# Optimization experiments

Hardware: AMD Instinct MI355X
Metric: run time of the kernel (lower is better)

Reference implementation:

```python
import jax, jax.numpy as jnp
from jax import lax
import numpy as np

POOLING_COUNTS = [15, 8, 8, 8]
N = 128          # segment_num
GROUPS = 4       # GroupNorm groups
TOPK = 5
NMS_THRESH = 0.5
EPS = 1e-5


def _build_structure(pooling_counts, n):
    """Static (numpy) replication of SparseMaxPool's mask2d and pooling schedule."""
    mask2d = np.zeros((n, n), dtype=bool)
    mask2d[np.arange(n), np.arange(n)] = True
    kinds = ['k2'] * pooling_counts[0]
    for c in pooling_counts[1:]:
        kinds += ['k3'] + ['k2'] * (c - 1)
    steps, stride, offset, k = [], 1, 0, 0
    for c in pooling_counts:
        for _ in range(c):
            offset += stride
            i = np.arange(0, n - offset, stride)
            j = np.arange(offset, n, stride)
            mask2d[i, j] = True
            steps.append((kinds[k], i, j))
            k += 1
        stride *= 2
    return mask2d, steps


_MASK2D, _STEPS = _build_structure(POOLING_COUNTS, N)


def sparse_max_pool(x):
    # x: [B, D, N] -> map2d: [B, D, N, N]
    B, D, _ = x.shape
    d = np.arange(N)
    map2d = jnp.zeros((B, D, N, N), x.dtype).at[:, :, d, d].set(x)
    for kind, i, j in _STEPS:
        if kind == 'k2':      # MaxPool1d(kernel=2, stride=1)
            x = jnp.maximum(x[..., :-1], x[..., 1:])
        else:                 # MaxPool1d(kernel=3, stride=2)
            m = jnp.maximum(jnp.maximum(x[..., :-2], x[..., 1:-1]), x[..., 2:])
            x = m[..., ::2]
        map2d = map2d.at[:, :, i, j].set(x)
    return map2d


def group_norm(x, gamma, beta):
    B, C, H, W = x.shape
    xg = x.reshape(B, GROUPS, C // GROUPS, H, W)
    mu = xg.mean(axis=(2, 3, 4), keepdims=True)
    var = xg.var(axis=(2, 3, 4), keepdims=True)
    xn = ((xg - mu) * lax.rsqrt(var + EPS)).reshape(B, C, H, W)
    return xn * gamma[None, :, None, None] + beta[None, :, None, None]


def decode(map2d, conv1_w, gn_gamma, gn_beta, conv2_w, conv2_b):
    dn = ('NCHW', 'OIHW', 'NCHW')
    h = lax.conv_general_dilated(map2d, conv1_w, (1, 1), [(1, 1), (1, 1)], dimension_numbers=dn)
    h = jax.nn.relu(group_norm(h, gn_gamma, gn_beta))
    out = lax.conv_general_dilated(h, conv2_w, (1, 1), [(0, 0), (0, 0)], dimension_numbers=dn)
    return out + conv2_b[None, :, None, None]


def greedy_nms(moments, scores):
    # moments: [M, 2] (start, end); scores: [M]
    M = moments.shape[0]
    order = jnp.argsort(-scores)
    m = moments[order]
    starts, ends = m[:, 0], m[:, 1]
    ar = jnp.arange(M)

    def body(i, sup):
        inter = jnp.clip(jnp.minimum(ends, ends[i]) - jnp.maximum(starts, starts[i]), 0.0)
        union = jnp.maximum(ends, ends[i]) - jnp.minimum(starts, starts[i])
        iou = inter / union
        newly = (iou > NMS_THRESH) & (ar > i) & jnp.logical_not(sup[i])
        return sup | newly

    sup = lax.fori_loop(0, M - 1, body, jnp.zeros((M,), bool))
    keep = jnp.logical_not(sup)
    # first TOPK kept rows in sorted order (static shape)
    pri = jnp.where(keep, M - ar, 0)
    _, idx = lax.top_k(pri, TOPK)
    return m[idx]


def reference(fea, duration, conv1_w, gn_gamma, gn_beta, conv2_w, conv2_b):
    map2d = sparse_max_pool(fea)
    out = decode(map2d, conv1_w, gn_gamma, gn_beta, conv2_w, conv2_b)
    mask = jnp.asarray(_MASK2D, out.dtype)
    score2d = (jax.nn.sigmoid(out) * mask)[0, 0]           # [N, N]
    # score2d_to_moments_scores: nonzero of masked map == static nonzero of mask2d
    gi, gj = np.nonzero(_MASK2D)                            # row-major, matches torch.nonzero
    scores = score2d[gi, gj]                                # [M]
    dur = float(duration)
    moments = jnp.asarray(
        np.stack([gi * (dur / N), (gj + 1) * (dur / N)], axis=-1), jnp.float32
    )                                                       # [M, 2]
    return greedy_nms(moments, scores)                      # [TOPK, 2]


def setup_inputs() -> dict:
    key = jax.random.key(0)
    k0, k1, k2 = jax.random.split(key, 3)
    D = 768
    return {
        'fea': jax.random.normal(k0, (1, D, N), jnp.float32),
        'duration': 30,
        'conv1_w': jax.random.normal(k1, (D, D, 3, 3), jnp.float32) * 0.02,
        'gn_gamma': jnp.ones((D,), jnp.float32),
        'gn_beta': jnp.zeros((D,), jnp.float32),
        'conv2_w': jax.random.normal(k2, (1, D, 1, 1), jnp.float32) * 0.02,
        'conv2_b': jnp.zeros((1,), jnp.float32),
    }
```

## Files before the change

### kernel.cpp

```cpp
#include <hip/hip_runtime.h>
#include <math.h>

#define NPIX 128
#define MASKM 2548
#define NPAD 2560
#define MG   6912
#define KD   768

typedef __attribute__((ext_vector_type(8))) short bf16x8;
typedef __attribute__((ext_vector_type(4))) float f32x4;
typedef __attribute__((ext_vector_type(16))) float f32x16;
typedef __attribute__((ext_vector_type(8))) unsigned short ushort8;

static constexpr size_t OFF_QI   = 0;
static constexpr size_t OFF_QJ   = OFF_QI + NPAD * 4;
static constexpr size_t OFF_QIDX = OFF_QJ + NPAD * 4;
static constexpr size_t OFF_APIX = OFF_QIDX + 16384 * 4;
static constexpr size_t OFF_BAR  = OFF_APIX + 16384 * 4;
static constexpr size_t OFF_LIST = OFF_BAR + 128 * 4;
static constexpr size_t OFF_PART = OFF_LIST + 16384 * 4;
static constexpr size_t OFF_SC   = OFF_PART + 512 * 8 * 8;
static constexpr size_t OFF_HM   = OFF_SC + NPAD * 4;
static constexpr size_t OFF_AH   = OFF_HM + (size_t)MASKM * KD * 4;
static constexpr size_t OFF_AL   = OFF_AH + (size_t)MG * KD * 2;
static constexpr size_t OFF_BH   = OFF_AL + (size_t)MG * KD * 2;
static constexpr size_t OFF_BL   = OFF_BH + (size_t)NPAD * KD * 2;
static constexpr size_t OFF_YT   = OFF_BL + (size_t)NPAD * KD * 2;

__device__ __forceinline__ unsigned short f2bf(float f) {
    unsigned u = __float_as_uint(f);
    u = u + 0x7FFFu + ((u >> 16) & 1u);
    return (unsigned short)(u >> 16);
}
__device__ __forceinline__ float bf2f(unsigned short h) {
    return __uint_as_float(((unsigned)h) << 16);
}

__device__ __forceinline__ bool mask_allowed(int i, int d) {
    if (d == 0) return true;
    if (d <= 15) return true;
    if (d <= 31) return (d >= 17) && ((d & 1) == 1) && ((i & 1) == 0);
    if (d <= 63) return (d >= 35) && ((d & 3) == 3) && ((i & 3) == 0);
    return (d >= 71) && ((d & 7) == 7) && ((i & 7) == 0);
}
__device__ __forceinline__ bool masked_ij(int i, int j) {
    return (j >= i) && (j < NPIX) && (i >= 0) && mask_allowed(i, j - i);
}

__device__ __forceinline__ int rank_to_d(int i, int r) {
    int rem = NPIX - i;
    int c1 = rem < 16 ? rem : 16;
    if (r < c1) return r;
    r -= c1;
    int h2 = (rem - 1) < 31 ? (rem - 1) : 31;
    int c2 = (((i & 1) == 0) && h2 >= 17) ? ((h2 - 17) >> 1) + 1 : 0;
    if (r < c2) return 17 + 2 * r;
    r -= c2;
    int h3 = (rem - 1) < 63 ? (rem - 1) : 63;
    int c3 = (((i & 3) == 0) && h3 >= 35) ? ((h3 - 35) >> 2) + 1 : 0;
    if (r < c3) return 35 + 4 * r;
    r -= c3;
    return 71 + 8 * r;
}

#define PREP_LDS 37888
#define PASTR 148

__global__ __launch_bounds__(256) void k_prep(const float* __restrict__ fea,
                                              const float* __restrict__ w1,
                                              int* __restrict__ qi, int* __restrict__ qj,
                                              int* __restrict__ qidx, int* __restrict__ apix,
                                              double* __restrict__ part, int* __restrict__ bar,
                                              int* __restrict__ list,
                                              unsigned short* __restrict__ Ah,
                                              unsigned short* __restrict__ Al,
                                              unsigned short* __restrict__ Bh,
                                              unsigned short* __restrict__ Bl) {
    extern __shared__ char smp[];
    int tid = threadIdx.x;
    int bid = blockIdx.x;

    if (bid < 64) {
        int* cnt = (int*)smp;
        int* startv = cnt + NPIX;
        if (tid < NPIX) {
            int c = 0;
            for (int d = 0; tid + d < NPIX; ++d) if (mask_allowed(tid, d)) ++c;
            cnt[tid] = c;
        }
        __syncthreads();
        if (tid == 0) {
            int s = 0;
            for (int r = 0; r < NPIX; ++r) { startv[r] = s; s += cnt[r]; }
        }
        __syncthreads();
        int p = bid * 256 + tid;
        int i = p >> 7, j = p & 127;
        int q = -1;
        if (masked_ij(i, j)) {
            int d = j - i, r = 0;
            for (int dd = 0; dd < d; ++dd) r += mask_allowed(i, dd) ? 1 : 0;
            q = startv[i] + r;
            qi[q] = i; qj[q] = j;
        }
        qidx[p] = q;
        int act = 0;
        #pragma unroll
        for (int dy = -1; dy <= 1; ++dy)
            #pragma unroll
            for (int dx = -1; dx <= 1; ++dx)
                if (masked_ij(i + dy, j + dx)) act = 1;
        apix[p] = act;
        if (act) { int idx = atomicAdd(&bar[3], 1); list[idx] = p; }
        if (bid == 0 && tid < 8) part[tid] = 0.0;
    } else if (bid < 160) {
        float* tab = (float*)smp;
        int* cnt = (int*)(smp + 32768);
        int* startv = (int*)(smp + 33280);
        int cb = bid - 64, c0 = cb * 8;
        if (tid < NPIX) {
            int c = 0;
            for (int d = 0; tid + d < NPIX; ++d) if (mask_allowed(tid, d)) ++c;
            cnt[tid] = c;
        }
        __syncthreads();
        if (tid == 0) {
            int s = 0;
            for (int r = 0; r < NPIX; ++r) { startv[r] = s; s += cnt[r]; }
            startv[NPIX] = s;
        }
        for (int idx = tid; idx < 8 * NPIX; idx += 256) {
            int c = idx >> 7, x = idx & 127;
            tab[(c * 8) * 128 + x] = fea[(size_t)(c0 + c) * NPIX + x];
        }
        __syncthreads();
        for (int lvl = 1; lvl < 8; ++lvl) {
            int half = 1 << (lvl - 1), full = 1 << lvl;
            for (int idx = tid; idx < 8 * NPIX; idx += 256) {
                int c = idx >> 7, x = idx & 127;
                if (x + full <= NPIX)
                    tab[(c * 8 + lvl) * 128 + x] =
                        fmaxf(tab[(c * 8 + lvl - 1) * 128 + x],
                              tab[(c * 8 + lvl - 1) * 128 + x + half]);
            }
            __syncthreads();
        }
        for (int q = tid; q < NPAD; q += 256) {
            ushort8 vh = {}, vl = {};
            if (q < MASKM) {
                int i = 0;
                #pragma unroll
                for (int s = 64; s >= 1; s >>= 1) {
                    int cand = i + s;
                    if (cand <= 127 && startv[cand] <= q) i = cand;
                }
                int d = rank_to_d(i, q - startv[i]);
                int j = i + d;
                int len = d + 1;
                int lvl = 31 - __clz(len);
                int x2 = j + 1 - (1 << lvl);
                #pragma unroll
                for (int c = 0; c < 8; ++c) {
                    float v = fmaxf(tab[(c * 8 + lvl) * 128 + i], tab[(c * 8 + lvl) * 128 + x2]);
                    unsigned short hh = f2bf(v);
                    vh[c] = hh; vl[c] = f2bf(v - bf2f(hh));
                }
            }
            *(ushort8*)(Bh + (size_t)q * KD + c0) = vh;
            *(ushort8*)(Bl + (size_t)q * KD + c0) = vl;
        }
    } else {
        float* tile = (float*)smp;
        int pb = bid - 160;
        int co0 = (pb % 12) * 64, ci0 = ((pb / 12) % 12) * 64;
        int s = pb / 144;
        int cib = ci0 + s * 16;
        for (int idx = tid; idx < 2304; idx += 256) {
            int row = idx / 36, c4 = idx % 36;
            float4 v = *(const float4*)(w1 + (size_t)(co0 + row) * MG + cib * 9 + c4 * 4);
            *(float4*)&tile[row * PASTR + c4 * 4] = v;
        }
        __syncthreads();
        for (int idx = tid; idx < 1152; idx += 256) {
            int tap = idx / 128;
            int rem = idx - tap * 128;
            int co = rem >> 1, half = rem & 1;
            ushort8 vh, vl;
            #pragma unroll
            for (int c = 0; c < 8; ++c) {
                float v = tile[co * PASTR + (half * 8 + c) * 9 + tap];
                unsigned short hi = f2bf(v);
                vh[c] = hi;
                vl[c] = f2bf(v - bf2f(hi));
            }
            size_t ob = (size_t)(tap * 768 + co0 + co) * KD + cib + half * 8;
            *(ushort8*)(Ah + ob) = vh;
            *(ushort8*)(Al + ob) = vl;
        }
    }
}

#define BUFSZ   73728
#define SB_BH   32768

__global__ __launch_bounds__(512, 1) void k_gemm(const unsigned short* __restrict__ Ah,
                                                 const unsigned short* __restrict__ Al,
                                                 const unsigned short* __restrict__ Bh,
                                                 const unsigned short* __restrict__ Bl,
                                                 float* __restrict__ Yt) {
    extern __shared__ char sm[];
    int tid = threadIdx.x;
    int wave = tid >> 6, lane = tid & 63;

    int bid = (int)blockIdx.x;
    int xcd = bid & 7, loc = bid >> 3;
    int m0 = loc * 256, n0 = xcd * 320;

    int wm = (wave & 3) << 6, wn = (wave >> 2) * 160;
    int r32 = lane & 31, hi2 = lane >> 5;
    int rb  = (r32 >> 4) * 1024 + hi2 * 256 + (r32 & 15) * 16;
    int awb = (wm >> 4) * 1024 + rb;
    int bwb = (wn >> 4) * 1024 + rb;

    int lrow = lane & 15, lchk = lane >> 4;
    const unsigned short* sp[9];
    int so[9];
    #pragma unroll
    for (int s = 0; s < 9; ++s) {
        int gid = wave * 9 + s;
        const unsigned short* base;
        int row0, ldso;
        if (gid < 16)      { base = Ah; row0 = m0 + gid * 16;        ldso = gid * 1024; }
        else if (gid < 32) { base = Al; row0 = m0 + (gid - 16) * 16; ldso = 16384 + (gid - 16) * 1024; }
        else if (gid < 52) { base = Bh; row0 = n0 + (gid - 32) * 16; ldso = SB_BH + (gid - 32) * 1024; }
        else               { base = Bl; row0 = n0 + (gid - 52) * 16; ldso = SB_BH + 20480 + (gid - 52) * 1024; }
        sp[s] = base + (size_t)(row0 + lrow) * KD + lchk * 8;
        so[s] = ldso;
    }

    f32x16 acc[2][5] = {};
    char* CB = sm;
    char* NB = sm + BUFSZ;

    #define STAGE(DST, s, koff) __builtin_amdgcn_global_load_lds( \
        (const __attribute__((address_space(1))) unsigned int*)(sp[s] + (koff)), \
        (__attribute__((address_space(3))) unsigned int*)((DST) + so[s]), 16, 0, 0)
    #define ARD(hl, mf, ks) (*(const bf16x8*)(CB + (hl) * 16384 + awb + (mf) * 2048 + (ks) * 512))
    #define BRD(hl, nf, ks) (*(const bf16x8*)(CB + SB_BH + (hl) * 20480 + bwb + (nf) * 2048 + (ks) * 512))
    #define TRIP(mf, nf, xh, xl, yh, yl) \
        acc[mf][nf] = __builtin_amdgcn_mfma_f32_32x32x16_bf16(xh, yh, acc[mf][nf], 0, 0, 0); \
        acc[mf][nf] = __builtin_amdgcn_mfma_f32_32x32x16_bf16(xh, yl, acc[mf][nf], 0, 0, 0); \
        acc[mf][nf] = __builtin_amdgcn_mfma_f32_32x32x16_bf16(xl, yh, acc[mf][nf], 0, 0, 0);
    #define RBAR __builtin_amdgcn_s_barrier()
    #define SB0  __builtin_amdgcn_sched_barrier(0)
    #define CL6(nf, xh0, xl0, xh1, xl1, yh, yl) \
        __builtin_amdgcn_s_setprio(1); \
        TRIP(0, nf, xh0, xl0, yh, yl) \
        TRIP(1, nf, xh1, xl1, yh, yl) \
        __builtin_amdgcn_s_setprio(0);

    #pragma unroll
    for (int s = 0; s < 9; ++s) STAGE(CB, s, 0);
    __syncthreads();

    for (int t = 0; t < 24; ++t) {
        int kn = (t + 1) * 32;
        bool stg = (t < 23);
        bf16x8 a0h, a0l, a1h, a1l;
        bf16x8 c0h, c0l, c1h, c1l;
        bf16x8 bxh, bxl, byh, byl;

        a0h = ARD(0, 0, 0); a0l = ARD(1, 0, 0);
        a1h = ARD(0, 1, 0); a1l = ARD(1, 1, 0);
        bxh = BRD(0, 0, 0); bxl = BRD(1, 0, 0);
        if (stg) { STAGE(NB, 0, kn); STAGE(NB, 1, kn); STAGE(NB, 2, kn); }
        RBAR;

        byh = BRD(0, 1, 0); byl = BRD(1, 1, 0);
        SB0;
        CL6(0, a0h, a0l, a1h, a1l, bxh, bxl)
        RBAR;
        bxh = BRD(0, 2, 0); bxl = BRD(1, 2, 0);
        SB0;
        CL6(1, a0h, a0l, a1h, a1l, byh, byl)
        RBAR;
        byh = BRD(0, 3, 0); byl = BRD(1, 3, 0);
        if (stg) { STAGE(NB, 3, kn); STAGE(NB, 4, kn); }
        SB0;
        CL6(2, a0h, a0l, a1h, a1l, bxh, bxl)
        RBAR;
        bxh = BRD(0, 4, 0); bxl = BRD(1, 4, 0);
        SB0;
        CL6(3, a0h, a0l, a1h, a1l, byh, byl)
        RBAR;
        c0h = ARD(0, 0, 1); c0l = ARD(1, 0, 1);
        c1h = ARD(0, 1, 1); c1l = ARD(1, 1, 1);
        byh = BRD(0, 0, 1); byl = BRD(1, 0, 1);
        if (stg) { STAGE(NB, 5, kn); STAGE(NB, 6, kn); }
        SB0;
        CL6(4, a0h, a0l, a1h, a1l, bxh, bxl)
        RBAR;
        bxh = BRD(0, 1, 1); bxl = BRD(1, 1, 1);
        SB0;
        CL6(0, c0h, c0l, c1h, c1l, byh, byl)
        RBAR;
        byh = BRD(0, 2, 1); byl = BRD(1, 2, 1);
        if (stg) { STAGE(NB, 7, kn); STAGE(NB, 8, kn); }
        SB0;
        CL6(1, c0h, c0l, c1h, c1l, bxh, bxl)
        RBAR;
        bxh = BRD(0, 3, 1); bxl = BRD(1, 3, 1);
        SB0;
        CL6(2, c0h, c0l, c1h, c1l, byh, byl)
        RBAR;
        byh = BRD(0, 4, 1); byl = BRD(1, 4, 1);
        SB0;
        CL6(3, c0h, c0l, c1h, c1l, bxh, bxl)
        RBAR;
        CL6(4, c0h, c0l, c1h, c1l, byh, byl)

        __syncthreads();
        char* tmp = CB; CB = NB; NB = tmp;
    }

    #pragma unroll
    for (int mf = 0; mf < 2; ++mf)
        #pragma unroll
        for (int nf = 0; nf < 5; ++nf) {
            int n = n0 + wn + nf * 32 + r32;
            size_t rowb = (size_t)n * MG + m0 + wm + mf * 32 + 4 * hi2;
            #pragma unroll
            for (int g = 0; g < 4; ++g) {
                f32x4 v = { acc[mf][nf][g * 4 + 0], acc[mf][nf][g * 4 + 1],
                            acc[mf][nf][g * 4 + 2], acc[mf][nf][g * 4 + 3] };
                *(f32x4*)(Yt + rowb + 8 * g) = v;
            }
        }
    #undef STAGE
    #undef ARD
    #undef BRD
    #undef TRIP
    #undef RBAR
    #undef SB0
    #undef CL6
}

__global__ __launch_bounds__(256) void k_gather(const float* __restrict__ Yt,
                                                const int* __restrict__ qidx,
                                                const int* __restrict__ list,
                                                const int* __restrict__ bar,
                                                float* __restrict__ hm,
                                                double* __restrict__ part) {
    __shared__ double red1[256 * 4], red2[256 * 4];
    int tid = threadIdx.x;
    int wave = tid >> 6, lane = tid & 63;
    double a1[3] = {0, 0, 0}, a2[3] = {0, 0, 0};
    int gs[3];
    #pragma unroll
    for (int s = 0; s < 3; ++s) gs[s] = (64 * s + lane) / 48;

    int nact = bar[3];
    for (int wid = blockIdx.x * 4 + wave; wid < nact; wid += gridDim.x * 4) {
        int p = list[wid];
        int y = p >> 7, x = p & 127;
        float4 hv[3] = {};
        #pragma unroll
        for (int tap = 0; tap < 9; ++tap) {
            int i = y + tap / 3 - 1, j = x + tap % 3 - 1;
            if ((unsigned)i < 128u && (unsigned)j < 128u) {
                int q = qidx[i * NPIX + j];
                if (q >= 0) {
                    const float* yr = Yt + (size_t)q * MG + tap * 768 + lane * 4;
                    #pragma unroll
                    for (int s = 0; s < 3; ++s) {
                        float4 v = *(const float4*)(yr + s * 256);
                        hv[s].x += v.x; hv[s].y += v.y; hv[s].z += v.z; hv[s].w += v.w;
                    }
                }
            }
        }
        int qp = qidx[p];
        if (qp >= 0) {
            #pragma unroll
            for (int s = 0; s < 3; ++s)
                *(float4*)(hm + (size_t)qp * KD + s * 256 + lane * 4) = hv[s];
        }
        #pragma unroll
        for (int s = 0; s < 3; ++s) {
            a1[s] += (double)hv[s].x + (double)hv[s].y + (double)hv[s].z + (double)hv[s].w;
            a2[s] += (double)hv[s].x * hv[s].x + (double)hv[s].y * hv[s].y +
                     (double)hv[s].z * hv[s].z + (double)hv[s].w * hv[s].w;
        }
    }
    #pragma unroll
    for (int g = 0; g < 4; ++g) { red1[tid * 4 + g] = 0.0; red2[tid * 4 + g] = 0.0; }
    #pragma unroll
    for (int s = 0; s < 3; ++s) { red1[tid * 4 + gs[s]] = a1[s]; red2[tid * 4 + gs[s]] = a2[s]; }
    __syncthreads();
    if (tid < 8) {
        int g = tid & 3;
        double s = 0.0;
        if (tid < 4) { for (int i = 0; i < 256; ++i) s += red1[i * 4 + g]; }
        else         { for (int i = 0; i < 256; ++i) s += red2[i * 4 + g]; }
        atomicAdd(&part[tid], s);
    }
}

#define SNMS_LDS 44544

__global__ __launch_bounds__(256) void k_scorenms(const float* __restrict__ hm,
                                                  const double* __restrict__ part,
                                                  const float* __restrict__ gamma,
                                                  const float* __restrict__ beta,
                                                  const float* __restrict__ w2,
                                                  const float* __restrict__ b2,
                                                  float* __restrict__ scores,
                                                  const int* __restrict__ qi,
                                                  const int* __restrict__ qj,
                                                  const int* __restrict__ durp,
                                                  int* __restrict__ bar,
                                                  float* __restrict__ out) {
    extern __shared__ char smf[];
    int tid = threadIdx.x;
    int bid = (int)blockIdx.x;
    int lane = tid & 63;

    {
        float mu[4], rs[4];
        const double cnt = 192.0 * 16384.0;
        #pragma unroll
        for (int g = 0; g < 4; ++g) {
            double m = part[g] / cnt;
            double v = part[4 + g] / cnt - m * m;
            mu[g] = (float)m;
            rs[g] = (float)(1.0 / sqrt(v + 1e-5));
        }
        int q = bid * 4 + (tid >> 6);
        const float* hp = hm + (size_t)q * KD;
        float s = 0.f;
        for (int c = lane; c < KD; c += 64) {
            int g = c / 192;
            float v = (hp[c] - mu[g]) * rs[g] * gamma[c] + beta[c];
            s += fmaxf(v, 0.f) * w2[c];
        }
        for (int o = 32; o; o >>= 1) s += __shfl_down(s, o, 64);
        if (lane == 0) scores[q] = 1.f / (1.f + expf(-(s + b2[0])));
    }
    __syncthreads();
    if (tid == 0)
        __hip_atomic_fetch_add(&bar[2], 1, __ATOMIC_RELEASE, __HIP_MEMORY_SCOPE_AGENT);
    if (bid != 0) return;

    if (tid == 0) {
        while (__hip_atomic_load(&bar[2], __ATOMIC_RELAXED, __HIP_MEMORY_SCOPE_AGENT) < 637)
            __builtin_amdgcn_s_sleep(8);
        (void)__hip_atomic_load(&bar[2], __ATOMIC_ACQUIRE, __HIP_MEMORY_SCOPE_AGENT);
    }
    __syncthreads();

    {
        unsigned long long* key = (unsigned long long*)smf;
        float* ss = (float*)(smf + 20384);
        float* ee = (float*)(smf + 30576);
        unsigned char* st = (unsigned char*)(smf + 40768);
        unsigned long long* wm0 = (unsigned long long*)(smf + 43328);
        unsigned long long* wm1 = (unsigned long long*)(smf + 43360);
        __shared__ int sh_keeper, keepq[5];
        __shared__ float sh_s0, sh_e0;

        float delta = (float)(*durp) / 128.f;
        for (int i = tid; i < MASKM; i += 256) {
            unsigned sb = __float_as_uint(scores[i]);
            key[i] = ((unsigned long long)sb << 32) | (unsigned)(4095 - i);
            ss[i] = qi[i] * delta;
            ee[i] = (qj[i] + 1) * delta;
            st[i] = 0;
        }
        __syncthreads();
        for (int round = 0; round < 5; ++round) {
            unsigned long long b0 = 0, b1 = 0;
            for (int i = tid; i < MASKM; i += 256) {
                unsigned char s = st[i];
                unsigned long long k = key[i];
                if (s == 0) { if (k > b0) b0 = k; }
                else if (s == 1) { if (k > b1) b1 = k; }
            }
            for (int o = 32; o; o >>= 1) {
                unsigned lo0 = __shfl_down((unsigned)b0, o, 64);
                unsigned hi0 = __shfl_down((unsigned)(b0 >> 32), o, 64);
                unsigned long long u0 = ((unsigned long long)hi0 << 32) | lo0;
                unsigned lo1 = __shfl_down((unsigned)b1, o, 64);
                unsigned hi1 = __shfl_down((unsigned)(b1 >> 32), o, 64);
                unsigned long long u1 = ((unsigned long long)hi1 << 32) | lo1;
                if (u0 > b0) b0 = u0;
                if (u1 > b1) b1 = u1;
            }
            if ((tid & 63) == 0) { wm0[tid >> 6] = b0; wm1[tid >> 6] = b1; }
            __syncthreads();
            if (tid == 0) {
                unsigned long long B0 = 0, B1 = 0;
                for (int w = 0; w < 4; ++w) {
                    if (wm0[w] > B0) B0 = wm0[w];
                    if (wm1[w] > B1) B1 = wm1[w];
                }
                int keeper = (B0 != 0);
                unsigned long long B = keeper ? B0 : B1;
                int q = 4095 - (int)(B & 0xFFFFFFFFull);
                st[q] = keeper ? 2 : 3;
                sh_keeper = keeper;
                sh_s0 = ss[q]; sh_e0 = ee[q];
                keepq[round] = q;
            }
            __syncthreads();
            if (sh_keeper) {
                float s0 = sh_s0, e0 = sh_e0;
                for (int i = tid; i < MASKM; i += 256) {
                    if (st[i] == 0) {
                        float inter = fminf(ee[i], e0) - fmaxf(ss[i], s0);
                        if (inter > 0.f) {
                            float uni = fmaxf(ee[i], e0) - fminf(ss[i], s0);
                            if (inter / uni > 0.5f) st[i] = 1;
                        }
                    }
                }
            }
            __syncthreads();
        }
        if (tid < 5) { out[tid * 2] = ss[keepq[tid]]; out[tid * 2 + 1] = ee[keepq[tid]]; }
    }
}

extern "C" void kernel_launch(void* const* d_in, const int* in_sizes, int n_in,
                              void* d_out, int out_size, void* d_ws, size_t ws_size,
                              hipStream_t stream) {
    const float* fea   = (const float*)d_in[0];
    const int*   dur   = (const int*)d_in[1];
    const float* w1    = (const float*)d_in[2];
    const float* gamma = (const float*)d_in[3];
    const float* beta  = (const float*)d_in[4];
    const float* w2    = (const float*)d_in[5];
    const float* b2    = (const float*)d_in[6];
    float* out = (float*)d_out;

    char* ws = (char*)d_ws;
    int*    qi     = (int*)(ws + OFF_QI);
    int*    qj     = (int*)(ws + OFF_QJ);
    int*    qidx   = (int*)(ws + OFF_QIDX);
    int*    apix   = (int*)(ws + OFF_APIX);
    int*    bar    = (int*)(ws + OFF_BAR);
    int*    list   = (int*)(ws + OFF_LIST);
    double* part   = (double*)(ws + OFF_PART);
    float*  scores = (float*)(ws + OFF_SC);
    float*  hm     = (float*)(ws + OFF_HM);
    unsigned short* AhU = (unsigned short*)(ws + OFF_AH);
    unsigned short* AlU = (unsigned short*)(ws + OFF_AL);
    unsigned short* BhU = (unsigned short*)(ws + OFF_BH);
    unsigned short* BlU = (unsigned short*)(ws + OFF_BL);
    float*  Yt     = (float*)(ws + OFF_YT);

    static bool attr_set = false;
    if (!attr_set) {
        hipFuncSetAttribute((const void*)k_prep,
                            hipFuncAttributeMaxDynamicSharedMemorySize, PREP_LDS);
        hipFuncSetAttribute((const void*)k_gemm,
                            hipFuncAttributeMaxDynamicSharedMemorySize, 2 * BUFSZ);
        hipFuncSetAttribute((const void*)k_scorenms,
                            hipFuncAttributeMaxDynamicSharedMemorySize, SNMS_LDS);
        attr_set = true;
    }

    hipMemsetAsync(bar, 0, 16, stream);
    k_prep<<<736, 256, PREP_LDS, stream>>>(fea, w1, qi, qj, qidx, apix, part, bar,
                                           list, AhU, AlU, BhU, BlU);
    k_gemm<<<216, 512, 2 * BUFSZ, stream>>>(AhU, AlU, BhU, BlU, Yt);
    k_gather<<<1536, 256, 0, stream>>>(Yt, qidx, list, bar, hm, part);
    k_scorenms<<<637, 256, SNMS_LDS, stream>>>(hm, part, gamma, beta, w2, b2,
                                               scores, qi, qj, dur, bar, out);
}
```

Measured before the change: 240.3 us.

## Fuse gather and score/NMS kernels with a grid barrier; closed-form mask ranks

```diff
diff --git a/kernel.cpp b/kernel.cpp
--- a/kernel.cpp
+++ b/kernel.cpp
@@ -15,8 +15,7 @@
 static constexpr size_t OFF_QI   = 0;
 static constexpr size_t OFF_QJ   = OFF_QI + NPAD * 4;
 static constexpr size_t OFF_QIDX = OFF_QJ + NPAD * 4;
-static constexpr size_t OFF_APIX = OFF_QIDX + 16384 * 4;
-static constexpr size_t OFF_BAR  = OFF_APIX + 16384 * 4;
+static constexpr size_t OFF_BAR  = OFF_QIDX + 16384 * 4;
 static constexpr size_t OFF_LIST = OFF_BAR + 128 * 4;
 static constexpr size_t OFF_PART = OFF_LIST + 16384 * 4;
 static constexpr size_t OFF_SC   = OFF_PART + 512 * 8 * 8;
@@ -47,6 +46,29 @@
     return (j >= i) && (j < NPIX) && (i >= 0) && mask_allowed(i, j - i);
 }
 
+__device__ __forceinline__ int row_cnt(int i) {
+    int rem = NPIX - i;
+    int c1 = rem < 16 ? rem : 16;
+    int h2 = (rem - 1) < 31 ? (rem - 1) : 31;
+    int c2 = (((i & 1) == 0) && h2 >= 17) ? ((h2 - 17) >> 1) + 1 : 0;
+    int h3 = (rem - 1) < 63 ? (rem - 1) : 63;
+    int c3 = (((i & 3) == 0) && h3 >= 35) ? ((h3 - 35) >> 2) + 1 : 0;
+    int h4 = rem - 1;
+    int c4 = (((i & 7) == 0) && h4 >= 71) ? ((h4 - 71) >> 3) + 1 : 0;
+    return c1 + c2 + c3 + c4;
+}
+__device__ __forceinline__ int rank_fwd(int i, int d) {
+    int rem = NPIX - i;
+    int c1 = rem < 16 ? rem : 16;
+    if (d < 16) return d;
+    int h2 = (rem - 1) < 31 ? (rem - 1) : 31;
+    int c2 = (((i & 1) == 0) && h2 >= 17) ? ((h2 - 17) >> 1) + 1 : 0;
+    if (d <= 31) return c1 + ((d - 17) >> 1);
+    int h3 = (rem - 1) < 63 ? (rem - 1) : 63;
+    int c3 = (((i & 3) == 0) && h3 >= 35) ? ((h3 - 35) >> 2) + 1 : 0;
+    if (d <= 63) return c1 + c2 + ((d - 35) >> 2);
+    return c1 + c2 + c3 + ((d - 71) >> 3);
+}
 __device__ __forceinline__ int rank_to_d(int i, int r) {
     int rem = NPIX - i;
     int c1 = rem < 16 ? rem : 16;
@@ -69,7 +91,7 @@
 __global__ __launch_bounds__(256) void k_prep(const float* __restrict__ fea,
                                               const float* __restrict__ w1,
                                               int* __restrict__ qi, int* __restrict__ qj,
-                                              int* __restrict__ qidx, int* __restrict__ apix,
+                                              int* __restrict__ qidx,
                                               double* __restrict__ part, int* __restrict__ bar,
                                               int* __restrict__ list,
                                               unsigned short* __restrict__ Ah,
@@ -81,52 +103,36 @@
     int bid = blockIdx.x;
 
     if (bid < 64) {
-        int* cnt = (int*)smp;
-        int* startv = cnt + NPIX;
-        if (tid < NPIX) {
-            int c = 0;
-            for (int d = 0; tid + d < NPIX; ++d) if (mask_allowed(tid, d)) ++c;
-            cnt[tid] = c;
-        }
-        __syncthreads();
+        int* startv = (int*)smp;
         if (tid == 0) {
             int s = 0;
-            for (int r = 0; r < NPIX; ++r) { startv[r] = s; s += cnt[r]; }
+            for (int r = 0; r < NPIX; ++r) { startv[r] = s; s += row_cnt(r); }
         }
         __syncthreads();
         int p = bid * 256 + tid;
         int i = p >> 7, j = p & 127;
-        int q = -1;
         if (masked_ij(i, j)) {
-            int d = j - i, r = 0;
-            for (int dd = 0; dd < d; ++dd) r += mask_allowed(i, dd) ? 1 : 0;
-            q = startv[i] + r;
+            int q = startv[i] + rank_fwd(i, j - i);
             qi[q] = i; qj[q] = j;
-        }
-        qidx[p] = q;
+            qidx[p] = q;
+        } else {
+            qidx[p] = -1;
+        }
         int act = 0;
         #pragma unroll
         for (int dy = -1; dy <= 1; ++dy)
             #pragma unroll
             for (int dx = -1; dx <= 1; ++dx)
                 if (masked_ij(i + dy, j + dx)) act = 1;
-        apix[p] = act;
         if (act) { int idx = atomicAdd(&bar[3], 1); list[idx] = p; }
         if (bid == 0 && tid < 8) part[tid] = 0.0;
     } else if (bid < 160) {
         float* tab = (float*)smp;
-        int* cnt = (int*)(smp + 32768);
-        int* startv = (int*)(smp + 33280);
+        int* startv = (int*)(smp + 32768);
         int cb = bid - 64, c0 = cb * 8;
-        if (tid < NPIX) {
-            int c = 0;
-            for (int d = 0; tid + d < NPIX; ++d) if (mask_allowed(tid, d)) ++c;
-            cnt[tid] = c;
-        }
-        __syncthreads();
         if (tid == 0) {
             int s = 0;
-            for (int r = 0; r < NPIX; ++r) { startv[r] = s; s += cnt[r]; }
+            for (int r = 0; r < NPIX; ++r) { startv[r] = s; s += row_cnt(r); }
             startv[NPIX] = s;
         }
         for (int idx = tid; idx < 8 * NPIX; idx += 256) {
@@ -345,85 +351,91 @@
     #undef CL6
 }
 
-__global__ __launch_bounds__(256) void k_gather(const float* __restrict__ Yt,
+#define GSN_LDS 44544
+
+__global__ __launch_bounds__(256, 3) void k_gsn(const float* __restrict__ Yt,
                                                 const int* __restrict__ qidx,
                                                 const int* __restrict__ list,
-                                                const int* __restrict__ bar,
+                                                const float* __restrict__ gamma,
+                                                const float* __restrict__ beta,
+                                                const float* __restrict__ w2,
+                                                const float* __restrict__ b2,
+                                                const int* __restrict__ qi,
+                                                const int* __restrict__ qj,
+                                                const int* __restrict__ durp,
+                                                double* __restrict__ part,
+                                                int* __restrict__ bar,
                                                 float* __restrict__ hm,
-                                                double* __restrict__ part) {
-    __shared__ double red1[256 * 4], red2[256 * 4];
-    int tid = threadIdx.x;
-    int wave = tid >> 6, lane = tid & 63;
-    double a1[3] = {0, 0, 0}, a2[3] = {0, 0, 0};
-    int gs[3];
-    #pragma unroll
-    for (int s = 0; s < 3; ++s) gs[s] = (64 * s + lane) / 48;
-
-    int nact = bar[3];
-    for (int wid = blockIdx.x * 4 + wave; wid < nact; wid += gridDim.x * 4) {
-        int p = list[wid];
-        int y = p >> 7, x = p & 127;
-        float4 hv[3] = {};
-        #pragma unroll
-        for (int tap = 0; tap < 9; ++tap) {
-            int i = y + tap / 3 - 1, j = x + tap % 3 - 1;
-            if ((unsigned)i < 128u && (unsigned)j < 128u) {
-                int q = qidx[i * NPIX + j];
-                if (q >= 0) {
-                    const float* yr = Yt + (size_t)q * MG + tap * 768 + lane * 4;
-                    #pragma unroll
-                    for (int s = 0; s < 3; ++s) {
-                        float4 v = *(const float4*)(yr + s * 256);
-                        hv[s].x += v.x; hv[s].y += v.y; hv[s].z += v.z; hv[s].w += v.w;
-                    }
-                }
-            }
-        }
-        int qp = qidx[p];
-        if (qp >= 0) {
-            #pragma unroll
-            for (int s = 0; s < 3; ++s)
-                *(float4*)(hm + (size_t)qp * KD + s * 256 + lane * 4) = hv[s];
-        }
-        #pragma unroll
-        for (int s = 0; s < 3; ++s) {
-            a1[s] += (double)hv[s].x + (double)hv[s].y + (double)hv[s].z + (double)hv[s].w;
-            a2[s] += (double)hv[s].x * hv[s].x + (double)hv[s].y * hv[s].y +
-                     (double)hv[s].z * hv[s].z + (double)hv[s].w * hv[s].w;
-        }
-    }
-    #pragma unroll
-    for (int g = 0; g < 4; ++g) { red1[tid * 4 + g] = 0.0; red2[tid * 4 + g] = 0.0; }
-    #pragma unroll
-    for (int s = 0; s < 3; ++s) { red1[tid * 4 + gs[s]] = a1[s]; red2[tid * 4 + gs[s]] = a2[s]; }
-    __syncthreads();
-    if (tid < 8) {
-        int g = tid & 3;
-        double s = 0.0;
-        if (tid < 4) { for (int i = 0; i < 256; ++i) s += red1[i * 4 + g]; }
-        else         { for (int i = 0; i < 256; ++i) s += red2[i * 4 + g]; }
-        atomicAdd(&part[tid], s);
-    }
-}
-
-#define SNMS_LDS 44544
-
-__global__ __launch_bounds__(256) void k_scorenms(const float* __restrict__ hm,
-                                                  const double* __restrict__ part,
-                                                  const float* __restrict__ gamma,
-                                                  const float* __restrict__ beta,
-                                                  const float* __restrict__ w2,
-                                                  const float* __restrict__ b2,
-                                                  float* __restrict__ scores,
-                                                  const int* __restrict__ qi,
-                                                  const int* __restrict__ qj,
-                                                  const int* __restrict__ durp,
-                                                  int* __restrict__ bar,
-                                                  float* __restrict__ out) {
+                                                float* __restrict__ scores,
+                                                float* __restrict__ out) {
     extern __shared__ char smf[];
     int tid = threadIdx.x;
     int bid = (int)blockIdx.x;
-    int lane = tid & 63;
+    int wave = tid >> 6, lane = tid & 63;
+
+    {
+        double* red1 = (double*)smf;
+        double* red2 = red1 + 1024;
+        double a1[3] = {0, 0, 0}, a2[3] = {0, 0, 0};
+        int gs[3];
+        #pragma unroll
+        for (int s = 0; s < 3; ++s) gs[s] = (64 * s + lane) / 48;
+
+        int nact = bar[3];
+        for (int wid = bid * 4 + wave; wid < nact; wid += 637 * 4) {
+            int p = list[wid];
+            int y = p >> 7, x = p & 127;
+            float4 hv[3] = {};
+            #pragma unroll
+            for (int tap = 0; tap < 9; ++tap) {
+                int i = y + tap / 3 - 1, j = x + tap % 3 - 1;
+                if ((unsigned)i < 128u && (unsigned)j < 128u) {
+                    int q = qidx[i * NPIX + j];
+                    if (q >= 0) {
+                        const float* yr = Yt + (size_t)q * MG + tap * 768 + lane * 4;
+                        #pragma unroll
+                        for (int s = 0; s < 3; ++s) {
+                            float4 v = *(const float4*)(yr + s * 256);
+                            hv[s].x += v.x; hv[s].y += v.y; hv[s].z += v.z; hv[s].w += v.w;
+                        }
+                    }
+                }
+            }
+            int qp = qidx[p];
+            if (qp >= 0) {
+                #pragma unroll
+                for (int s = 0; s < 3; ++s)
+                    *(float4*)(hm + (size_t)qp * KD + s * 256 + lane * 4) = hv[s];
+            }
+            #pragma unroll
+            for (int s = 0; s < 3; ++s) {
+                a1[s] += (double)hv[s].x + (double)hv[s].y + (double)hv[s].z + (double)hv[s].w;
+                a2[s] += (double)hv[s].x * hv[s].x + (double)hv[s].y * hv[s].y +
+                         (double)hv[s].z * hv[s].z + (double)hv[s].w * hv[s].w;
+            }
+        }
+        #pragma unroll
+        for (int g = 0; g < 4; ++g) { red1[tid * 4 + g] = 0.0; red2[tid * 4 + g] = 0.0; }
+        #pragma unroll
+        for (int s = 0; s < 3; ++s) { red1[tid * 4 + gs[s]] = a1[s]; red2[tid * 4 + gs[s]] = a2[s]; }
+        __syncthreads();
+        if (tid < 8) {
+            int g = tid & 3;
+            double s = 0.0;
+            if (tid < 4) { for (int i = 0; i < 256; ++i) s += red1[i * 4 + g]; }
+            else         { for (int i = 0; i < 256; ++i) s += red2[i * 4 + g]; }
+            atomicAdd(&part[tid], s);
+        }
+    }
+
+    __syncthreads();
+    if (tid == 0) {
+        __hip_atomic_fetch_add(&bar[0], 1, __ATOMIC_RELEASE, __HIP_MEMORY_SCOPE_AGENT);
+        while (__hip_atomic_load(&bar[0], __ATOMIC_RELAXED, __HIP_MEMORY_SCOPE_AGENT) < 637)
+            __builtin_amdgcn_s_sleep(8);
+        (void)__hip_atomic_load(&bar[0], __ATOMIC_ACQUIRE, __HIP_MEMORY_SCOPE_AGENT);
+    }
+    __syncthreads();
 
     {
         float mu[4], rs[4];
@@ -435,7 +447,7 @@
             mu[g] = (float)m;
             rs[g] = (float)(1.0 / sqrt(v + 1e-5));
         }
-        int q = bid * 4 + (tid >> 6);
+        int q = bid * 4 + wave;
         const float* hp = hm + (size_t)q * KD;
         float s = 0.f;
         for (int c = lane; c < KD; c += 64) {
@@ -448,13 +460,13 @@
     }
     __syncthreads();
     if (tid == 0)
-        __hip_atomic_fetch_add(&bar[2], 1, __ATOMIC_RELEASE, __HIP_MEMORY_SCOPE_AGENT);
+        __hip_atomic_fetch_add(&bar[1], 1, __ATOMIC_RELEASE, __HIP_MEMORY_SCOPE_AGENT);
     if (bid != 0) return;
 
     if (tid == 0) {
-        while (__hip_atomic_load(&bar[2], __ATOMIC_RELAXED, __HIP_MEMORY_SCOPE_AGENT) < 637)
+        while (__hip_atomic_load(&bar[1], __ATOMIC_RELAXED, __HIP_MEMORY_SCOPE_AGENT) < 637)
             __builtin_amdgcn_s_sleep(8);
-        (void)__hip_atomic_load(&bar[2], __ATOMIC_ACQUIRE, __HIP_MEMORY_SCOPE_AGENT);
+        (void)__hip_atomic_load(&bar[1], __ATOMIC_ACQUIRE, __HIP_MEMORY_SCOPE_AGENT);
     }
     __syncthreads();
 
@@ -546,7 +558,6 @@
     int*    qi     = (int*)(ws + OFF_QI);
     int*    qj     = (int*)(ws + OFF_QJ);
     int*    qidx   = (int*)(ws + OFF_QIDX);
-    int*    apix   = (int*)(ws + OFF_APIX);
     int*    bar    = (int*)(ws + OFF_BAR);
     int*    list   = (int*)(ws + OFF_LIST);
     double* part   = (double*)(ws + OFF_PART);
@@ -564,16 +575,15 @@
                             hipFuncAttributeMaxDynamicSharedMemorySize, PREP_LDS);
         hipFuncSetAttribute((const void*)k_gemm,
                             hipFuncAttributeMaxDynamicSharedMemorySize, 2 * BUFSZ);
-        hipFuncSetAttribute((const void*)k_scorenms,
-                            hipFuncAttributeMaxDynamicSharedMemorySize, SNMS_LDS);
+        hipFuncSetAttribute((const void*)k_gsn,
+                            hipFuncAttributeMaxDynamicSharedMemorySize, GSN_LDS);
         attr_set = true;
     }
 
     hipMemsetAsync(bar, 0, 16, stream);
-    k_prep<<<736, 256, PREP_LDS, stream>>>(fea, w1, qi, qj, qidx, apix, part, bar,
+    k_prep<<<736, 256, PREP_LDS, stream>>>(fea, w1, qi, qj, qidx, part, bar,
                                            list, AhU, AlU, BhU, BlU);
     k_gemm<<<216, 512, 2 * BUFSZ, stream>>>(AhU, AlU, BhU, BlU, Yt);
-    k_gather<<<1536, 256, 0, stream>>>(Yt, qidx, list, bar, hm, part);
-    k_scorenms<<<637, 256, SNMS_LDS, stream>>>(hm, part, gamma, beta, w2, b2,
-                                               scores, qi, qj, dur, bar, out);
-}
+    k_gsn<<<637, 256, GSN_LDS, stream>>>(Yt, qidx, list, gamma, beta, w2, b2,
+                                         qi, qj, dur, part, bar, hm, scores, out);
+}
```

After: 279.7 us. 16.4% more time.
